# Kernel optimization log

Hardware: AMD Instinct MI355X
Metric: run time of the kernel (lower is better)

## Reference

```python
import jax, jax.numpy as jnp
import numpy as np

EMBED_DIM = 1024
NUM_HEADS = 16
HEAD_DIM = EMBED_DIM // NUM_HEADS
B, S = 2, 2048


def setup_inputs() -> dict:
    key = jax.random.key(0)
    k = jax.random.split(key, 8)
    scale = 1.0 / np.sqrt(EMBED_DIM)
    return {
        "x": jax.random.normal(k[0], (B, S, EMBED_DIM), dtype=jnp.float32),
        "x1": jax.random.normal(k[1], (B, S, EMBED_DIM), dtype=jnp.float32),
        "x2": jax.random.normal(k[2], (B, S, EMBED_DIM), dtype=jnp.float32),
        "qkv_w": jax.random.normal(k[3], (3 * EMBED_DIM, EMBED_DIM), dtype=jnp.float32) * scale,
        "qkv_b": jnp.zeros((3 * EMBED_DIM,), dtype=jnp.float32),
        "out_w": jax.random.normal(k[4], (EMBED_DIM, EMBED_DIM), dtype=jnp.float32) * scale,
        "out_b": jnp.zeros((EMBED_DIM,), dtype=jnp.float32),
    }


def reference(x, x1, x2, qkv_w, qkv_b, out_w, out_b):
    # x1, x2 are accepted but unused, matching the torch module.
    b, s, e = x.shape
    qkv = x @ qkv_w.T + qkv_b                      # [B,S,3E]
    qkv = qkv.reshape(b, s, 3, NUM_HEADS, HEAD_DIM)
    qkv = jnp.transpose(qkv, (2, 0, 3, 1, 4))      # [3,B,H,S,D]
    q, k, v = qkv[0], qkv[1], qkv[2]
    scores = jnp.einsum("bhqd,bhkd->bhqk", q, k) / np.sqrt(HEAD_DIM)
    probs = jax.nn.sigmoid(scores)                 # [B,H,S,S]
    sample = jax.random.bernoulli(jax.random.key(42), probs).astype(probs.dtype)
    # straight-through: forward uses sample, gradient flows as identity to probs
    attn = probs + jax.lax.stop_gradient(sample - probs)
    out = jnp.einsum("bhqk,bhkd->bhqd", attn, v)   # [B,H,S,D]
    out = jnp.transpose(out, (0, 2, 1, 3)).reshape(b, s, e)
    return out @ out_w.T + out_b
```

## Files before the change

kernel.cpp:

```cpp
#include <hip/hip_runtime.h>
#include <stdint.h>

#define NB 2
#define NS 2048
#define NE 1024
#define NH 16
#define ND 64

typedef __attribute__((ext_vector_type(8))) short short8;
typedef __attribute__((ext_vector_type(4))) float f4;
typedef __attribute__((ext_vector_type(16))) float f16v;
typedef __attribute__((ext_vector_type(4))) unsigned short us4;

static __device__ __forceinline__ unsigned short bf16_rne(float x) {
  uint32_t u = __builtin_bit_cast(uint32_t, x);
  u += 0x7fffu + ((u >> 16) & 1u);
  return (unsigned short)(u >> 16);
}
static __device__ __forceinline__ float bf16_f32(unsigned short h) {
  uint32_t u = ((uint32_t)h) << 16;
  return __builtin_bit_cast(float, u);
}

static __device__ __forceinline__ void threefry42(uint32_t x0, uint32_t x1,
                                                  uint32_t& o0, uint32_t& o1) {
  const uint32_t ks0 = 0u, ks1 = 42u;
  const uint32_t ks2 = 0u ^ 42u ^ 0x1BD11BDAu;
  x0 += ks0; x1 += ks1;
#define TF4(a,b,c,d) \
  x0 += x1; x1 = __builtin_rotateleft32(x1, a); x1 ^= x0; \
  x0 += x1; x1 = __builtin_rotateleft32(x1, b); x1 ^= x0; \
  x0 += x1; x1 = __builtin_rotateleft32(x1, c); x1 ^= x0; \
  x0 += x1; x1 = __builtin_rotateleft32(x1, d); x1 ^= x0;
  TF4(13,15,26,6)  x0 += ks1; x1 += ks2 + 1u;
  TF4(17,29,16,24) x0 += ks2; x1 += ks0 + 2u;
  TF4(13,15,26,6)  x0 += ks0; x1 += ks1 + 3u;
  TF4(17,29,16,24) x0 += ks1; x1 += ks2 + 4u;
  TF4(13,15,26,6)  x0 += ks2; x1 += ks0 + 5u;
#undef TF4
  o0 = x0; o1 = x1;
}

static __device__ __forceinline__ void gl2lds16(const void* g, void* l) {
  __builtin_amdgcn_global_load_lds(
      (const __attribute__((address_space(1))) uint32_t*)g,
      (__attribute__((address_space(3))) uint32_t*)l, 16, 0, 0);
}

__global__ void k_split(const float* __restrict__ x, const float* __restrict__ qw,
                        const float* __restrict__ ow,
                        unsigned short* __restrict__ xh, unsigned short* __restrict__ xl,
                        unsigned short* __restrict__ wh, unsigned short* __restrict__ wl,
                        unsigned short* __restrict__ woh) {
  for (uint32_t i = blockIdx.x * 256u + threadIdx.x; i < 8388608u; i += gridDim.x * 256u) {
    if (i < 4194304u) {
      float v = x[i];
      unsigned short hi = bf16_rne(v);
      xh[i] = hi;
      xl[i] = bf16_rne(v - bf16_f32(hi));
    } else if (i < 7340032u) {
      uint32_t j = i - 4194304u;
      float v = qw[j];
      unsigned short hi = bf16_rne(v);
      wh[j] = hi;
      wl[j] = bf16_rne(v - bf16_f32(hi));
    } else {
      uint32_t j = i - 7340032u;
      woh[j] = bf16_rne(ow[j]);
    }
  }
}

__global__ __launch_bounds__(256) void k_qkv(
    const unsigned short* __restrict__ xh, const unsigned short* __restrict__ xl,
    const unsigned short* __restrict__ wh, const unsigned short* __restrict__ wl,
    const float* __restrict__ qkv_b,
    unsigned short* __restrict__ Qh, unsigned short* __restrict__ Ql,
    unsigned short* __restrict__ Kh, unsigned short* __restrict__ Kl,
    unsigned short* __restrict__ Vt) {
  __shared__ unsigned short SM[16384];
  unsigned short* Ah = SM;
  unsigned short* Al = SM + 4096;
  unsigned short* Bh = SM + 8192;
  unsigned short* Bl = SM + 12288;
  const int tid = threadIdx.x;
  const int lane = tid & 63, wid = tid >> 6;
  const int wm = wid >> 1, wn = wid & 1;
  const int bn = blockIdx.x, bm = blockIdx.y;
  const bool isV = (bn >= 16);
  const int l31 = lane & 31, h = lane >> 5;
  const int ldrow = lane >> 2;
  const int ldk = (((lane & 3) - ((lane >> 3) & 3)) & 3) * 8;
  const int rot = (l31 >> 1) & 3;

  f16v acc[2][2];
#pragma unroll
  for (int a = 0; a < 2; ++a)
#pragma unroll
    for (int b = 0; b < 2; ++b)
      acc[a][b] = (f16v){0.f,0.f,0.f,0.f,0.f,0.f,0.f,0.f,0.f,0.f,0.f,0.f,0.f,0.f,0.f,0.f};

  for (int kt = 0; kt < 32; ++kt) {
    const int k0 = kt * 32;
    __syncthreads();
#pragma unroll
    for (int r = 0; r < 2; ++r) {
      const int c = wid + r * 4;
      const int grow = c * 16 + ldrow;
      const size_t ao = (size_t)(bm * 128 + grow) * 1024 + k0 + ldk;
      const size_t bo = (size_t)(bn * 128 + grow) * 1024 + k0 + ldk;
      const int lo = c * 512 + lane * 8;
      gl2lds16(xh + ao, &Ah[lo]);
      gl2lds16(wh + bo, &Bh[lo]);
      if (!isV) {
        gl2lds16(xl + ao, &Al[lo]);
        gl2lds16(wl + bo, &Bl[lo]);
      }
    }
    __syncthreads();

#pragma unroll
    for (int ks = 0; ks < 2; ++ks) {
      const int lc = ks * 2 + h;
      const int pcs = ((lc + rot) & 3) * 8;
      short8 af[2], bf_[2], alf[2], blf[2];
#pragma unroll
      for (int t = 0; t < 2; ++t) {
        const int arow = wm * 64 + t * 32 + l31;
        const int brow = wn * 64 + t * 32 + l31;
        af[t]  = *(const short8*)&Ah[arow * 32 + pcs];
        bf_[t] = *(const short8*)&Bh[brow * 32 + pcs];
        if (!isV) {
          alf[t] = *(const short8*)&Al[arow * 32 + pcs];
          blf[t] = *(const short8*)&Bl[brow * 32 + pcs];
        }
      }
      if (isV) {
#pragma unroll
        for (int tm = 0; tm < 2; ++tm)
#pragma unroll
          for (int tn = 0; tn < 2; ++tn)
            acc[tm][tn] = __builtin_amdgcn_mfma_f32_32x32x16_bf16(af[tm], bf_[tn], acc[tm][tn], 0, 0, 0);
      } else {
#pragma unroll
        for (int tm = 0; tm < 2; ++tm)
#pragma unroll
          for (int tn = 0; tn < 2; ++tn) {
            acc[tm][tn] = __builtin_amdgcn_mfma_f32_32x32x16_bf16(af[tm], bf_[tn], acc[tm][tn], 0, 0, 0);
            acc[tm][tn] = __builtin_amdgcn_mfma_f32_32x32x16_bf16(af[tm], blf[tn], acc[tm][tn], 0, 0, 0);
            acc[tm][tn] = __builtin_amdgcn_mfma_f32_32x32x16_bf16(alf[tm], bf_[tn], acc[tm][tn], 0, 0, 0);
          }
      }
    }
  }

  if (!isV) {
#pragma unroll
    for (int tm = 0; tm < 2; ++tm) {
#pragma unroll
      for (int tn = 0; tn < 2; ++tn) {
        const int j = bn * 128 + wn * 64 + tn * 32 + l31;
        const float bias = qkv_b[j];
        const int which = j >> 10;
        const int rem = j & 1023;
        const int hd = rem >> 6, d = rem & 63;
#pragma unroll
        for (int a = 0; a < 16; ++a) {
          const int m_local = wm * 64 + tm * 32 + (a & 3) + 8 * (a >> 2) + 4 * h;
          const int i = bm * 128 + m_local;
          const int b = i >> 11, s = i & 2047;
          const size_t off = (((size_t)(b * 16 + hd)) * 2048 + (size_t)s) * 64 + d;
          const float v = acc[tm][tn][a] + bias;
          const unsigned short hi = bf16_rne(v);
          const unsigned short lo = bf16_rne(v - bf16_f32(hi));
          if (which == 0) { Qh[off] = hi; Ql[off] = lo; }
          else            { Kh[off] = hi; Kl[off] = lo; }
        }
      }
    }
  } else {
    __syncthreads();
#pragma unroll
    for (int tm = 0; tm < 2; ++tm) {
#pragma unroll
      for (int tn = 0; tn < 2; ++tn) {
        const int d_local = wn * 64 + tn * 32 + l31;
        const float bias = qkv_b[bn * 128 + d_local];
#pragma unroll
        for (int a = 0; a < 16; ++a) {
          const int s_local = wm * 64 + tm * 32 + (a & 3) + 8 * (a >> 2) + 4 * h;
          SM[d_local * 128 + s_local] = bf16_rne(acc[tm][tn][a] + bias);
        }
      }
    }
    __syncthreads();
    const int b = (bm * 128) >> 11;
    const int s0 = (bm * 128) & 2047;
    const int h2 = (bn - 16) * 2;
#pragma unroll
    for (int it = 0; it < 8; ++it) {
      const int chunk = it * 256 + tid;
      const int dr = chunk >> 4;
      const int sc = (chunk & 15) * 8;
      const short8 v = *(const short8*)&SM[dr * 128 + sc];
      const int bh = b * 16 + h2 + (dr >> 6);
      const int d = dr & 63;
      *(short8*)&Vt[((size_t)bh * 64 + d) * 2048 + s0 + sc] = v;
    }
  }
}

__global__ __launch_bounds__(256) void k_attn(
    const unsigned short* __restrict__ Qh, const unsigned short* __restrict__ Ql,
    const unsigned short* __restrict__ Khg, const unsigned short* __restrict__ Klg,
    const unsigned short* __restrict__ Vtg, unsigned short* __restrict__ AO) {
  __shared__ unsigned short Ksh[4096], Ksl[4096], Vs[8192], Pm[4096];
  const int tid = threadIdx.x;
  const int lane = tid & 63, w = tid >> 6;
  const int quad = lane >> 4, c16 = lane & 15;
  const int q0 = blockIdx.x * 64;
  const int bh = blockIdx.y;
  const size_t base = (size_t)bh * (size_t)(2048 * 64);

  const size_t qoff = base + (size_t)(q0 + w * 16 + c16) * 64 + quad * 8;
  const short8 qh0 = *(const short8*)&Qh[qoff];
  const short8 qh1 = *(const short8*)&Qh[qoff + 32];
  const short8 ql0 = *(const short8*)&Ql[qoff];
  const short8 ql1 = *(const short8*)&Ql[qoff + 32];

  const uint32_t fb = (uint32_t)bh * 4194304u +
                      (uint32_t)(q0 + w * 16 + quad * 4) * 2048u + (uint32_t)c16;

  const int c0 = tid, r0 = c0 >> 3, g0 = ((c0 & 7) - r0) & 7;
  const int c1 = tid + 256, r1 = c1 >> 3, g1 = ((c1 & 7) - r1) & 7;

  f4 oacc[4];
#pragma unroll
  for (int s = 0; s < 4; ++s) { f4 z = {0.f, 0.f, 0.f, 0.f}; oacc[s] = z; }

  auto stage = [&](int kb, int vbuf) {
    const size_t koff = base + (size_t)kb * 64;
    gl2lds16(Khg + koff + r0 * 64 + g0 * 8, &Ksh[c0 * 8]);
    gl2lds16(Klg + koff + r0 * 64 + g0 * 8, &Ksl[c0 * 8]);
    gl2lds16(Vtg + base + (size_t)r0 * 2048 + kb + g0 * 8, &Vs[vbuf * 4096 + c0 * 8]);
    gl2lds16(Khg + koff + r1 * 64 + g1 * 8, &Ksh[c1 * 8]);
    gl2lds16(Klg + koff + r1 * 64 + g1 * 8, &Ksl[c1 * 8]);
    gl2lds16(Vtg + base + (size_t)r1 * 2048 + kb + g1 * 8, &Vs[vbuf * 4096 + c1 * 8]);
  };

  stage(0, 0);

  for (int kt = 0; kt < 32; ++kt) {
    const int kb = kt * 64;
    const int vb = (kt & 1) * 4096;
    __syncthreads();

    f4 sacc[4];
#pragma unroll
    for (int sub = 0; sub < 4; ++sub) {
      const int rK = sub * 16 + c16;
      const int sA = ((quad + rK) & 7) * 8;
      const int sB = ((quad + 4 + rK) & 7) * 8;
      const short8 kh0 = *(const short8*)&Ksh[rK * 64 + sA];
      const short8 kh1 = *(const short8*)&Ksh[rK * 64 + sB];
      const short8 kl0 = *(const short8*)&Ksl[rK * 64 + sA];
      const short8 kl1 = *(const short8*)&Ksl[rK * 64 + sB];
      f4 s = {0.f, 0.f, 0.f, 0.f};
      s = __builtin_amdgcn_mfma_f32_16x16x32_bf16(qh0, kh0, s, 0, 0, 0);
      s = __builtin_amdgcn_mfma_f32_16x16x32_bf16(qh1, kh1, s, 0, 0, 0);
      s = __builtin_amdgcn_mfma_f32_16x16x32_bf16(qh0, kl0, s, 0, 0, 0);
      s = __builtin_amdgcn_mfma_f32_16x16x32_bf16(qh1, kl1, s, 0, 0, 0);
      s = __builtin_amdgcn_mfma_f32_16x16x32_bf16(ql0, kh0, s, 0, 0, 0);
      s = __builtin_amdgcn_mfma_f32_16x16x32_bf16(ql1, kh1, s, 0, 0, 0);
      sacc[sub] = s;
    }
    __syncthreads();
    if (kt < 31) stage(kb + 64, (kt & 1) ^ 1);

#pragma unroll
    for (int sub = 0; sub < 4; ++sub) {
      const int qP = sub * 2 + (c16 >> 3);
#pragma unroll
      for (int rr = 0; rr < 4; ++rr) {
        const uint32_t f = fb + (uint32_t)(rr * 2048) + (uint32_t)(kb + sub * 16);
        uint32_t o0, o1;
        threefry42(0u, f, o0, o1);
        const float m = (float)((o0 ^ o1) >> 9);
        const float e = __builtin_amdgcn_exp2f(sacc[sub][rr] * -0.18033688f);
        const int rP = w * 16 + quad * 4 + rr;
        const int addr = rP * 64 + (((qP + rP) & 7) * 8) + (c16 & 7);
        Pm[addr] = (fmaf(m, e, m) < 8388608.0f) ? 0x3F80u : 0u;
      }
    }

    const int rp = w * 16 + c16;
    const short8 pa0 = *(const short8*)&Pm[rp * 64 + ((quad + rp) & 7) * 8];
    const short8 pa1 = *(const short8*)&Pm[rp * 64 + ((quad + 4 + rp) & 7) * 8];
#pragma unroll
    for (int sub = 0; sub < 4; ++sub) {
      const int rV = sub * 16 + c16;
      const short8 vv0 = *(const short8*)&Vs[vb + rV * 64 + ((quad + rV) & 7) * 8];
      const short8 vv1 = *(const short8*)&Vs[vb + rV * 64 + ((quad + 4 + rV) & 7) * 8];
      oacc[sub] = __builtin_amdgcn_mfma_f32_16x16x32_bf16(pa0, vv0, oacc[sub], 0, 0, 0);
      oacc[sub] = __builtin_amdgcn_mfma_f32_16x16x32_bf16(pa1, vv1, oacc[sub], 0, 0, 0);
    }
  }

  const int b = bh >> 4, hh = bh & 15;
#pragma unroll
  for (int sub = 0; sub < 4; ++sub)
#pragma unroll
    for (int r = 0; r < 4; ++r) {
      const int srow = b * 2048 + q0 + w * 16 + quad * 4 + r;
      AO[(size_t)srow * 1024 + hh * 64 + sub * 16 + c16] = bf16_rne(oacc[sub][r]);
    }
}

__global__ __launch_bounds__(256) void k_out(
    const unsigned short* __restrict__ A, const unsigned short* __restrict__ Bw,
    const float* __restrict__ out_b, float* __restrict__ out) {
  __shared__ unsigned short As[128 * 32], Bs[128 * 32];
  const int tid = threadIdx.x;
  const int lane = tid & 63, wid = tid >> 6;
  const int wm = wid >> 1, wn = wid & 1;
  const int bn = blockIdx.x, bm = blockIdx.y;
  const int l31 = lane & 31, h = lane >> 5;
  const int ldrow = lane >> 2;
  const int ldk = (((lane & 3) - ((lane >> 3) & 3)) & 3) * 8;
  const int rot = (l31 >> 1) & 3;

  f16v acc[2][2];
#pragma unroll
  for (int a = 0; a < 2; ++a)
#pragma unroll
    for (int b = 0; b < 2; ++b)
      acc[a][b] = (f16v){0.f,0.f,0.f,0.f,0.f,0.f,0.f,0.f,0.f,0.f,0.f,0.f,0.f,0.f,0.f,0.f};

  for (int kt = 0; kt < 32; ++kt) {
    const int k0 = kt * 32;
    __syncthreads();
#pragma unroll
    for (int r = 0; r < 2; ++r) {
      const int c = wid + r * 4;
      const int grow = c * 16 + ldrow;
      const size_t ao = (size_t)(bm * 128 + grow) * 1024 + k0 + ldk;
      const size_t bo = (size_t)(bn * 128 + grow) * 1024 + k0 + ldk;
      const int lo = c * 512 + lane * 8;
      gl2lds16(A + ao, &As[lo]);
      gl2lds16(Bw + bo, &Bs[lo]);
    }
    __syncthreads();

#pragma unroll
    for (int ks = 0; ks < 2; ++ks) {
      const int lc = ks * 2 + h;
      const int pcs = ((lc + rot) & 3) * 8;
      short8 af[2], bf_[2];
#pragma unroll
      for (int t = 0; t < 2; ++t) {
        af[t]  = *(const short8*)&As[(wm * 64 + t * 32 + l31) * 32 + pcs];
        bf_[t] = *(const short8*)&Bs[(wn * 64 + t * 32 + l31) * 32 + pcs];
      }
#pragma unroll
      for (int tm = 0; tm < 2; ++tm)
#pragma unroll
        for (int tn = 0; tn < 2; ++tn)
          acc[tm][tn] = __builtin_amdgcn_mfma_f32_32x32x16_bf16(af[tm], bf_[tn], acc[tm][tn], 0, 0, 0);
    }
  }

#pragma unroll
  for (int tm = 0; tm < 2; ++tm) {
#pragma unroll
    for (int tn = 0; tn < 2; ++tn) {
      const int j = bn * 128 + wn * 64 + tn * 32 + l31;
      const float bias = out_b[j];
#pragma unroll
      for (int a = 0; a < 16; ++a) {
        const int i = bm * 128 + wm * 64 + tm * 32 + (a & 3) + 8 * (a >> 2) + 4 * h;
        out[(size_t)i * 1024 + j] = acc[tm][tn][a] + bias;
      }
    }
  }
}

extern "C" void kernel_launch(void* const* d_in, const int* in_sizes, int n_in,
                              void* d_out, int out_size, void* d_ws, size_t ws_size,
                              hipStream_t stream) {
  const float* x     = (const float*)d_in[0];
  const float* qkv_w = (const float*)d_in[3];
  const float* qkv_b = (const float*)d_in[4];
  const float* out_w = (const float*)d_in[5];
  const float* out_b = (const float*)d_in[6];
  float* out = (float*)d_out;

  unsigned short* xh  = (unsigned short*)d_ws;
  unsigned short* xl  = xh + 4194304;
  unsigned short* wh  = xl + 4194304;
  unsigned short* wl  = wh + 3145728;
  unsigned short* woh = wl + 3145728;
  unsigned short* Vt  = woh + 1048576;
  unsigned short* Qh  = Vt + 4194304;
  unsigned short* Ql  = Qh + 4194304;
  unsigned short* Kh  = Ql + 4194304;
  unsigned short* Kl  = Kh + 4194304;
  unsigned short* AO  = xh;

  k_split<<<8192, 256, 0, stream>>>(x, qkv_w, out_w, xh, xl, wh, wl, woh);
  k_qkv<<<dim3(24, 32), 256, 0, stream>>>(xh, xl, wh, wl, qkv_b, Qh, Ql, Kh, Kl, Vt);
  k_attn<<<dim3(32, 32), 256, 0, stream>>>(Qh, Ql, Kh, Kl, Vt, AO);
  k_out<<<dim3(8, 32), 256, 0, stream>>>(AO, woh, out_b, out);
}
```

Baseline: 502.7 us.

## Double-buffer LDS tiles in QKV and output projection GEMMs

Both projection GEMM kernels now use two LDS buffers. The loads for tile k+1 are issued right after the barrier and before the MFMA work on tile k, so only one barrier per iteration is needed. The goal is to hide global-to-LDS load latency behind matrix math. In exchange, the QKV kernel's LDS footprint doubles to 64 KB, which may cut occupancy, and the attention kernel is left unchanged.

```diff
diff --git a/kernel.cpp b/kernel.cpp
--- a/kernel.cpp
+++ b/kernel.cpp
@@ -78,11 +78,7 @@
     unsigned short* __restrict__ Qh, unsigned short* __restrict__ Ql,
     unsigned short* __restrict__ Kh, unsigned short* __restrict__ Kl,
     unsigned short* __restrict__ Vt) {
-  __shared__ unsigned short SM[16384];
-  unsigned short* Ah = SM;
-  unsigned short* Al = SM + 4096;
-  unsigned short* Bh = SM + 8192;
-  unsigned short* Bl = SM + 12288;
+  __shared__ unsigned short SM[32768];
   const int tid = threadIdx.x;
   const int lane = tid & 63, wid = tid >> 6;
   const int wm = wid >> 1, wn = wid & 1;
@@ -100,9 +96,9 @@
     for (int b = 0; b < 2; ++b)
       acc[a][b] = (f16v){0.f,0.f,0.f,0.f,0.f,0.f,0.f,0.f,0.f,0.f,0.f,0.f,0.f,0.f,0.f,0.f};
 
-  for (int kt = 0; kt < 32; ++kt) {
+  auto stage = [&](int kt, int buf) {
     const int k0 = kt * 32;
-    __syncthreads();
+    unsigned short* Ah = SM + buf * 16384;
 #pragma unroll
     for (int r = 0; r < 2; ++r) {
       const int c = wid + r * 4;
@@ -111,14 +107,25 @@
       const size_t bo = (size_t)(bn * 128 + grow) * 1024 + k0 + ldk;
       const int lo = c * 512 + lane * 8;
       gl2lds16(xh + ao, &Ah[lo]);
-      gl2lds16(wh + bo, &Bh[lo]);
+      gl2lds16(wh + bo, &Ah[8192 + lo]);
       if (!isV) {
-        gl2lds16(xl + ao, &Al[lo]);
-        gl2lds16(wl + bo, &Bl[lo]);
-      }
-    }
-    __syncthreads();
-
+        gl2lds16(xl + ao, &Ah[4096 + lo]);
+        gl2lds16(wl + bo, &Ah[12288 + lo]);
+      }
+    }
+  };
+
+  stage(0, 0);
+
+  for (int kt = 0; kt < 32; ++kt) {
+    const int cb = kt & 1;
+    __syncthreads();
+    if (kt < 31) stage(kt + 1, cb ^ 1);
+
+    const unsigned short* Ah = SM + cb * 16384;
+    const unsigned short* Al = Ah + 4096;
+    const unsigned short* Bh = Ah + 8192;
+    const unsigned short* Bl = Ah + 12288;
 #pragma unroll
     for (int ks = 0; ks < 2; ++ks) {
       const int lc = ks * 2 + h;
@@ -319,7 +326,7 @@
 __global__ __launch_bounds__(256) void k_out(
     const unsigned short* __restrict__ A, const unsigned short* __restrict__ Bw,
     const float* __restrict__ out_b, float* __restrict__ out) {
-  __shared__ unsigned short As[128 * 32], Bs[128 * 32];
+  __shared__ unsigned short SM[16384];
   const int tid = threadIdx.x;
   const int lane = tid & 63, wid = tid >> 6;
   const int wm = wid >> 1, wn = wid & 1;
@@ -336,9 +343,9 @@
     for (int b = 0; b < 2; ++b)
       acc[a][b] = (f16v){0.f,0.f,0.f,0.f,0.f,0.f,0.f,0.f,0.f,0.f,0.f,0.f,0.f,0.f,0.f,0.f};
 
-  for (int kt = 0; kt < 32; ++kt) {
+  auto stage = [&](int kt, int buf) {
     const int k0 = kt * 32;
-    __syncthreads();
+    unsigned short* As = SM + buf * 8192;
 #pragma unroll
     for (int r = 0; r < 2; ++r) {
       const int c = wid + r * 4;
@@ -347,10 +354,19 @@
       const size_t bo = (size_t)(bn * 128 + grow) * 1024 + k0 + ldk;
       const int lo = c * 512 + lane * 8;
       gl2lds16(A + ao, &As[lo]);
-      gl2lds16(Bw + bo, &Bs[lo]);
-    }
-    __syncthreads();
-
+      gl2lds16(Bw + bo, &As[4096 + lo]);
+    }
+  };
+
+  stage(0, 0);
+
+  for (int kt = 0; kt < 32; ++kt) {
+    const int cb = kt & 1;
+    __syncthreads();
+    if (kt < 31) stage(kt + 1, cb ^ 1);
+
+    const unsigned short* As = SM + cb * 8192;
+    const unsigned short* Bs = As + 4096;
 #pragma unroll
     for (int ks = 0; ks < 2; ++ks) {
       const int lc = ks * 2 + h;
```

Result: no change. 502.7 us (-0.0%).
